# Optimization experiments

Hardware: AMD Instinct MI355X
Metric: run time of the kernel (lower is better)

Reference implementation:

```python
import jax, jax.numpy as jnp
import numpy as np

BINS = 10  # constructor default


def setup_inputs() -> dict:
    key = jax.random.key(0)
    k1, k2 = jax.random.split(key)
    bs, cla = 262144, 128
    # probabilities strictly inside (0,1) so log terms are finite
    u = jax.random.uniform(k1, (bs, cla), dtype=jnp.float32)
    inputs = 0.01 + 0.98 * u
    # binary 0/1 targets as floats
    targets = jnp.round(jax.random.uniform(k2, (bs, cla), dtype=jnp.float32))
    return {"inputs": inputs, "targets": targets}


def reference(inputs, targets):
    bins = BINS
    tot = jnp.asarray(inputs.size, jnp.float32)  # bs * cla

    # gradient-norm proxy g = |p.detach() - t|, in [0, 1]
    g = jnp.abs(jax.lax.stop_gradient(inputs) - targets)

    # edges are i/bins with the last edge nudged to 1+1e-6, so
    # floor(g*bins) clipped to bins-1 reproduces the per-bin masks exactly
    idx = jnp.clip(jnp.floor(g * bins).astype(jnp.int32), 0, bins - 1)

    # histogram counts per bin (fused scatter-add instead of the Python loop)
    counts = jnp.zeros((bins,), jnp.float32).at[idx.ravel()].add(1.0)

    n = jnp.sum(counts > 0).astype(jnp.float32)  # number of non-empty bins
    w_per_bin = jnp.where(counts > 0, tot / jnp.maximum(counts, 1.0), 0.0)
    weights = w_per_bin[idx] / jnp.maximum(n, 1.0)
    weights = jax.lax.stop_gradient(weights)  # weights built from detached g

    # elementwise binary cross entropy on probabilities
    bce = -(targets * jnp.log(inputs) + (1.0 - targets) * jnp.log1p(-inputs))
    loss = jnp.sum(weights * bce) / tot
    return loss
```

## Files before the change

kernel.cpp:

```cpp
#include <hip/hip_runtime.h>

#define BINS 10

__global__ __launch_bounds__(256) void ghm_partial(
    const float4* __restrict__ p4,
    const float4* __restrict__ t4,
    float* __restrict__ gsum,
    unsigned int* __restrict__ gcnt,
    int n4)
{
    __shared__ float ls[BINS];
    __shared__ float lc[BINS];
    const int tid = threadIdx.x;
    if (tid < BINS) { ls[tid] = 0.0f; lc[tid] = 0.0f; }
    __syncthreads();

    float sums[BINS];
    float cnts[BINS];
#pragma unroll
    for (int b = 0; b < BINS; ++b) { sums[b] = 0.0f; cnts[b] = 0.0f; }

    const int start  = blockIdx.x * blockDim.x + threadIdx.x;
    const int stride = gridDim.x * blockDim.x;

    for (int i = start; i < n4; i += stride) {
        float4 p = p4[i];
        float4 t = t4[i];
        float pe[4] = {p.x, p.y, p.z, p.w};
        float te[4] = {t.x, t.y, t.z, t.w};
#pragma unroll
        for (int e = 0; e < 4; ++e) {
            float pp = pe[e], tt = te[e];
            float g = fabsf(pp - tt);
            float q = (tt > 0.5f) ? pp : (1.0f - pp);
            float bce = -__logf(q);
            int bi = (int)(g * 10.0f);
            bi = bi > (BINS - 1) ? (BINS - 1) : bi;
#pragma unroll
            for (int b = 0; b < BINS; ++b) {
                bool m = (bi == b);
                sums[b] += m ? bce  : 0.0f;
                cnts[b] += m ? 1.0f : 0.0f;
            }
        }
    }

    const int lane = threadIdx.x & 63;
#pragma unroll
    for (int b = 0; b < BINS; ++b) {
        float s = sums[b], c = cnts[b];
#pragma unroll
        for (int off = 32; off > 0; off >>= 1) {
            s += __shfl_down(s, off);
            c += __shfl_down(c, off);
        }
        if (lane == 0) {
            atomicAdd(&ls[b], s);
            atomicAdd(&lc[b], c);
        }
    }
    __syncthreads();
    if (tid < BINS) {
        atomicAdd(&gsum[tid], ls[tid]);
        atomicAdd(&gcnt[tid], (unsigned int)lc[tid]);
    }
}

__global__ void ghm_finalize(const float* __restrict__ gsum,
                             const unsigned int* __restrict__ gcnt,
                             float* __restrict__ out)
{
    if (threadIdx.x == 0 && blockIdx.x == 0) {
        int n = 0;
#pragma unroll
        for (int b = 0; b < BINS; ++b) n += (gcnt[b] > 0) ? 1 : 0;
        float nn = (float)(n > 0 ? n : 1);
        float acc = 0.0f;
#pragma unroll
        for (int b = 0; b < BINS; ++b) {
            if (gcnt[b] > 0)
                acc += gsum[b] / ((float)gcnt[b] * nn);
        }
        out[0] = acc;
    }
}

extern "C" void kernel_launch(void* const* d_in, const int* in_sizes, int n_in,
                              void* d_out, int out_size, void* d_ws, size_t ws_size,
                              hipStream_t stream)
{
    const float* p = (const float*)d_in[0];
    const float* t = (const float*)d_in[1];
    const int n  = in_sizes[0];
    const int n4 = n >> 2;

    float*        gsum = (float*)d_ws;
    unsigned int* gcnt = (unsigned int*)((char*)d_ws + BINS * sizeof(float));

    hipMemsetAsync(d_ws, 0, BINS * (sizeof(float) + sizeof(unsigned int)), stream);

    const int threads = 256;
    const int blocks  = 2048;
    ghm_partial<<<blocks, threads, 0, stream>>>(
        (const float4*)p, (const float4*)t, gsum, gcnt, n4);

    ghm_finalize<<<1, 64, 0, stream>>>(gsum, gcnt, (float*)d_out);
}
```

Baseline: 314.4 us.

## Replace per-thread bin registers with lane-private shared-memory histograms via LDS atomics

Drops the 10-way masked register accumulation and the per-bin wavefront shuffle reductions. Each element instead does LDS atomic adds into a per-lane histogram copy, padded to stride 11 to spread banks, and the 64 copies are summed at block end. It also simplifies the BCE to -log(1-g) and unrolls the main loop. The cost is two LDS atomics per element, shared by the 4 waves that use the same per-lane copy, which may serialize more than the register selects they replace.

```diff
diff --git a/kernel.cpp b/kernel.cpp
--- a/kernel.cpp
+++ b/kernel.cpp
@@ -1,6 +1,8 @@
 #include <hip/hip_runtime.h>
 
 #define BINS 10
+#define COPIES 64
+#define HSTRIDE 11
 
 __global__ __launch_bounds__(256) void ghm_partial(
     const float4* __restrict__ p4,
@@ -9,60 +11,71 @@
     unsigned int* __restrict__ gcnt,
     int n4)
 {
-    __shared__ float ls[BINS];
-    __shared__ float lc[BINS];
+    __shared__ float        s_sum[COPIES * HSTRIDE];
+    __shared__ unsigned int s_cnt[COPIES * HSTRIDE];
+
     const int tid = threadIdx.x;
-    if (tid < BINS) { ls[tid] = 0.0f; lc[tid] = 0.0f; }
+    for (int k = tid; k < COPIES * HSTRIDE; k += 256) {
+        s_sum[k] = 0.0f;
+        s_cnt[k] = 0u;
+    }
     __syncthreads();
 
-    float sums[BINS];
-    float cnts[BINS];
-#pragma unroll
-    for (int b = 0; b < BINS; ++b) { sums[b] = 0.0f; cnts[b] = 0.0f; }
+    const int lane_base = (tid & 63) * HSTRIDE;
+    const int start  = blockIdx.x * blockDim.x + tid;
+    const int stride = gridDim.x * blockDim.x;
+    const int iters  = n4 / stride;
 
-    const int start  = blockIdx.x * blockDim.x + threadIdx.x;
-    const int stride = gridDim.x * blockDim.x;
-
-    for (int i = start; i < n4; i += stride) {
+    int i = start;
+#pragma unroll 4
+    for (int it = 0; it < iters; ++it, i += stride) {
         float4 p = p4[i];
         float4 t = t4[i];
         float pe[4] = {p.x, p.y, p.z, p.w};
         float te[4] = {t.x, t.y, t.z, t.w};
 #pragma unroll
         for (int e = 0; e < 4; ++e) {
-            float pp = pe[e], tt = te[e];
-            float g = fabsf(pp - tt);
-            float q = (tt > 0.5f) ? pp : (1.0f - pp);
-            float bce = -__logf(q);
-            int bi = (int)(g * 10.0f);
+            float g   = fabsf(pe[e] - te[e]);
+            float bce = -__logf(1.0f - g);
+            int   bi  = (int)(g * 10.0f);
             bi = bi > (BINS - 1) ? (BINS - 1) : bi;
+            int idx = lane_base + bi;
+            __hip_atomic_fetch_add(&s_sum[idx], bce, __ATOMIC_RELAXED,
+                                   __HIP_MEMORY_SCOPE_WORKGROUP);
+            __hip_atomic_fetch_add(&s_cnt[idx], 1u, __ATOMIC_RELAXED,
+                                   __HIP_MEMORY_SCOPE_WORKGROUP);
+        }
+    }
+    for (int j = iters * stride + start; j < n4; j += stride) {
+        float4 p = p4[j];
+        float4 t = t4[j];
+        float pe[4] = {p.x, p.y, p.z, p.w};
+        float te[4] = {t.x, t.y, t.z, t.w};
 #pragma unroll
-            for (int b = 0; b < BINS; ++b) {
-                bool m = (bi == b);
-                sums[b] += m ? bce  : 0.0f;
-                cnts[b] += m ? 1.0f : 0.0f;
-            }
+        for (int e = 0; e < 4; ++e) {
+            float g   = fabsf(pe[e] - te[e]);
+            float bce = -__logf(1.0f - g);
+            int   bi  = (int)(g * 10.0f);
+            bi = bi > (BINS - 1) ? (BINS - 1) : bi;
+            int idx = lane_base + bi;
+            __hip_atomic_fetch_add(&s_sum[idx], bce, __ATOMIC_RELAXED,
+                                   __HIP_MEMORY_SCOPE_WORKGROUP);
+            __hip_atomic_fetch_add(&s_cnt[idx], 1u, __ATOMIC_RELAXED,
+                                   __HIP_MEMORY_SCOPE_WORKGROUP);
         }
     }
 
-    const int lane = threadIdx.x & 63;
-#pragma unroll
-    for (int b = 0; b < BINS; ++b) {
-        float s = sums[b], c = cnts[b];
-#pragma unroll
-        for (int off = 32; off > 0; off >>= 1) {
-            s += __shfl_down(s, off);
-            c += __shfl_down(c, off);
-        }
-        if (lane == 0) {
-            atomicAdd(&ls[b], s);
-            atomicAdd(&lc[b], c);
-        }
-    }
     __syncthreads();
     if (tid < BINS) {
-        atomicAdd(&gsum[tid], ls[tid]);
-        atomicAdd(&gcnt[tid], (unsigned int)lc[tid]);
+        float s = 0.0f;
+        for (int l = 0; l < COPIES; ++l) s += s_sum[l * HSTRIDE + tid];
+        atomicAdd(&gsum[tid], s);
+    }
+    if (tid >= 16 && tid < 16 + BINS) {
+        const int b = tid - 16;
+        unsigned int c = 0u;
+        for (int l = 0; l < COPIES; ++l) c += s_cnt[l * HSTRIDE + b];
+        atomicAdd(&gcnt[b], c);
     }
 }
 
```

Result: slower. 362.7 us (+15.4%).

## Use log(1-g) BCE identity, ballot-based bin counts and software-pipelined loads

Applied to the files above, without the earlier changes.

The per-element BCE becomes log2(1-g), relying on the targets being binary, and the ln2 scale and sign move into the finalize kernel. This drops the per-element select and the natural-log scaling. Per-bin counts are now taken with a wave ballot and popcount into wave-uniform integer counters, which removes the per-bin float count accumulation and its shuffle reduction. The main loop is software-pipelined two iterations deep with two float4 loads per input, and launch bounds ask for 4 blocks per CU. The clamp on the bin index is removed, so an element with g equal to 1 would index out of range.

```diff
diff --git a/kernel.cpp b/kernel.cpp
--- a/kernel.cpp
+++ b/kernel.cpp
@@ -2,67 +2,102 @@
 
 #define BINS 10
 
-__global__ __launch_bounds__(256) void ghm_partial(
+__device__ __forceinline__ void elem(float p, float t,
+                                     float* __restrict__ sb,
+                                     unsigned int* __restrict__ cw)
+{
+    float g  = fabsf(p - t);
+    float l2 = __log2f(1.0f - g);
+    int   bi = (int)(g * 10.0f);
+#pragma unroll
+    for (int b = 0; b < BINS; ++b) {
+        bool hit = (bi == b);
+        unsigned long long m = __ballot(hit);
+        sb[b] += hit ? l2 : 0.0f;
+        cw[b] += (unsigned int)__popcll(m);
+    }
+}
+
+__device__ __forceinline__ void proc8(const float4 pa, const float4 pb,
+                                      const float4 ta, const float4 tb,
+                                      float* __restrict__ sb,
+                                      unsigned int* __restrict__ cw)
+{
+    elem(pa.x, ta.x, sb, cw); elem(pa.y, ta.y, sb, cw);
+    elem(pa.z, ta.z, sb, cw); elem(pa.w, ta.w, sb, cw);
+    elem(pb.x, tb.x, sb, cw); elem(pb.y, tb.y, sb, cw);
+    elem(pb.z, tb.z, sb, cw); elem(pb.w, tb.w, sb, cw);
+}
+
+__global__ __launch_bounds__(256, 4) void ghm_partial(
     const float4* __restrict__ p4,
     const float4* __restrict__ t4,
     float* __restrict__ gsum,
     unsigned int* __restrict__ gcnt,
     int n4)
 {
-    __shared__ float ls[BINS];
-    __shared__ float lc[BINS];
-    const int tid = threadIdx.x;
-    if (tid < BINS) { ls[tid] = 0.0f; lc[tid] = 0.0f; }
+    float        sb[BINS];
+    unsigned int cw[BINS];
+#pragma unroll
+    for (int b = 0; b < BINS; ++b) { sb[b] = 0.0f; cw[b] = 0u; }
+
+    const int tid     = threadIdx.x;
+    const int start   = blockIdx.x * blockDim.x + tid;
+    const int stride  = gridDim.x * blockDim.x;
+    const int stride2 = 2 * stride;
+    const int nouter  = n4 / stride2;
+
+    if (nouter >= 2) {
+        int i = start;
+        float4 pa0 = p4[i], pb0 = p4[i + stride];
+        float4 ta0 = t4[i], tb0 = t4[i + stride];
+        i += stride2;
+        float4 pa1 = p4[i], pb1 = p4[i + stride];
+        float4 ta1 = t4[i], tb1 = t4[i + stride];
+        i += stride2;
+        for (int it = 0; it < nouter - 2; ++it, i += stride2) {
+            float4 na = p4[i], nb = p4[i + stride];
+            float4 ma = t4[i], mb = t4[i + stride];
+            proc8(pa0, pb0, ta0, tb0, sb, cw);
+            pa0 = pa1; pb0 = pb1; ta0 = ta1; tb0 = tb1;
+            pa1 = na;  pb1 = nb;  ta1 = ma;  tb1 = mb;
+        }
+        proc8(pa0, pb0, ta0, tb0, sb, cw);
+        proc8(pa1, pb1, ta1, tb1, sb, cw);
+    } else {
+        for (int k = 0; k < 2 * nouter; ++k) {
+            int i = start + k * stride;
+            float4 p = p4[i], t = t4[i];
+            elem(p.x, t.x, sb, cw); elem(p.y, t.y, sb, cw);
+            elem(p.z, t.z, sb, cw); elem(p.w, t.w, sb, cw);
+        }
+    }
+    for (int j = start + nouter * stride2; j < n4; j += stride) {
+        float4 p = p4[j], t = t4[j];
+        elem(p.x, t.x, sb, cw); elem(p.y, t.y, sb, cw);
+        elem(p.z, t.z, sb, cw); elem(p.w, t.w, sb, cw);
+    }
+
+    __shared__ float        redS[BINS];
+    __shared__ unsigned int redC[BINS];
+    if (tid < BINS) { redS[tid] = 0.0f; redC[tid] = 0u; }
     __syncthreads();
 
-    float sums[BINS];
-    float cnts[BINS];
-#pragma unroll
-    for (int b = 0; b < BINS; ++b) { sums[b] = 0.0f; cnts[b] = 0.0f; }
-
-    const int start  = blockIdx.x * blockDim.x + threadIdx.x;
-    const int stride = gridDim.x * blockDim.x;
-
-    for (int i = start; i < n4; i += stride) {
-        float4 p = p4[i];
-        float4 t = t4[i];
-        float pe[4] = {p.x, p.y, p.z, p.w};
-        float te[4] = {t.x, t.y, t.z, t.w};
-#pragma unroll
-        for (int e = 0; e < 4; ++e) {
-            float pp = pe[e], tt = te[e];
-            float g = fabsf(pp - tt);
-            float q = (tt > 0.5f) ? pp : (1.0f - pp);
-            float bce = -__logf(q);
-            int bi = (int)(g * 10.0f);
-            bi = bi > (BINS - 1) ? (BINS - 1) : bi;
-#pragma unroll
-            for (int b = 0; b < BINS; ++b) {
-                bool m = (bi == b);
-                sums[b] += m ? bce  : 0.0f;
-                cnts[b] += m ? 1.0f : 0.0f;
-            }
-        }
-    }
-
-    const int lane = threadIdx.x & 63;
+    const int lane = tid & 63;
 #pragma unroll
     for (int b = 0; b < BINS; ++b) {
-        float s = sums[b], c = cnts[b];
+        float s = sb[b];
 #pragma unroll
-        for (int off = 32; off > 0; off >>= 1) {
-            s += __shfl_down(s, off);
-            c += __shfl_down(c, off);
-        }
+        for (int off = 32; off > 0; off >>= 1) s += __shfl_down(s, off);
         if (lane == 0) {
-            atomicAdd(&ls[b], s);
-            atomicAdd(&lc[b], c);
+            atomicAdd(&redS[b], s);
+            atomicAdd(&redC[b], cw[b]);
         }
     }
     __syncthreads();
     if (tid < BINS) {
-        atomicAdd(&gsum[tid], ls[tid]);
-        atomicAdd(&gcnt[tid], (unsigned int)lc[tid]);
+        atomicAdd(&gsum[tid], redS[tid]);
+        atomicAdd(&gcnt[tid], redC[tid]);
     }
 }
 
@@ -73,15 +108,15 @@
     if (threadIdx.x == 0 && blockIdx.x == 0) {
         int n = 0;
 #pragma unroll
-        for (int b = 0; b < BINS; ++b) n += (gcnt[b] > 0) ? 1 : 0;
+        for (int b = 0; b < BINS; ++b) n += (gcnt[b] > 0u) ? 1 : 0;
         float nn = (float)(n > 0 ? n : 1);
         float acc = 0.0f;
 #pragma unroll
         for (int b = 0; b < BINS; ++b) {
-            if (gcnt[b] > 0)
+            if (gcnt[b] > 0u)
                 acc += gsum[b] / ((float)gcnt[b] * nn);
         }
-        out[0] = acc;
+        out[0] = -0.6931471805599453f * acc;
     }
 }
 
```

Result: faster. 293.0 us (-6.8%).
